# Kernel tuning notes

Hardware: AMD Instinct MI355X
Metric: run time of the kernel (lower is better)

Reference implementation:

```python
import math
import jax, jax.numpy as jnp
import numpy as np

# ---- static config (matches init_kwargs) ----
IN_CH, OUT_CH = 32, 32
NR, NPHI = 3, 4                      # kernel_shape
H, W = 1024, 1024                    # in_shape
KSIZE = (NR - 1) * NPHI + 1          # 9
RC = 2.0 * NR / float(max(H, W))     # default radius_cutoff
S = math.floor(2 * RC * max(H, W) / 2) + 1  # psi_local_size = 7


def _compute_psi_loc() -> np.ndarray:
    """Numpy replica of _precompute_convolution_tensor_2d + scatter into psi_loc."""
    dr = RC / NR
    dphi = 2.0 * np.pi / NPHI
    ik = np.arange(KSIZE).reshape(-1, 1, 1)            # (K,1,1)
    ir = ((ik - 1) // NPHI + 1) * dr                   # floor-div matches torch
    iphi = ((ik - 1) % NPHI) * dphi
    # local grid of offsets, grid_out = origin
    lin = np.linspace(-RC, RC, S)
    X, Y = np.meshgrid(lin, lin, indexing='ij')        # torch.meshgrid default 'ij'
    dx = X.reshape(1, -1)                              # diffs[0], (1, S*S)
    dy = Y.reshape(1, -1)
    r = np.sqrt(dx ** 2 + dy ** 2)                     # (1, S*S)
    phi = np.arctan2(dy, dx) + np.pi
    # norm='2d'
    norm = (np.pi * (RC * NR / (NR + 1)) ** 2
            + np.pi * RC ** 2 * (2 * NR / (NR + 1) + 1) / (NR + 1) / 3)
    cond_r = (np.abs(r - ir) <= dr) & (r <= RC)        # (K,1,S*S)
    dph = np.abs(phi - iphi)
    cond_phi = (ik == 0) | (dph <= dphi) | (2 * np.pi - dph <= dphi)
    f_idx, _, j_idx = np.nonzero(cond_r & cond_phi)
    rv, phv = r[0, j_idx], phi[0, j_idx]
    irv, iphv = ir[f_idx, 0, 0], iphi[f_idx, 0, 0]
    vals = (1.0 - np.abs(rv - irv) / dr) / norm
    d = np.abs(phv - iphv)
    vals = vals * np.where(f_idx > 0, 1.0 - np.minimum(d, 2 * np.pi - d) / dphi, 1.0)
    psi = np.zeros((KSIZE, S * S), dtype=np.float32)
    psi[f_idx, j_idx] = vals.astype(np.float32)        # unique (f,j) pairs -> set
    psi = psi.reshape(KSIZE, S, S) * (4.0 / float(H * W))
    return psi


def setup_inputs() -> dict:
    key = jax.random.key(0)
    kx, kw = jax.random.split(key)
    x = jax.random.normal(kx, (4, IN_CH, H, W), dtype=jnp.float32)
    scale = math.sqrt(1.0 / IN_CH)  # groups=1 -> groupsize = in_channels
    weight = scale * jax.random.normal(kw, (OUT_CH, IN_CH, KSIZE), dtype=jnp.float32)
    bias = jnp.zeros((OUT_CH,), dtype=jnp.float32)
    psi_loc = jnp.asarray(_compute_psi_loc())
    return {"x": x, "weight": weight, "bias": bias, "psi_loc": psi_loc}


def reference(x, weight, bias, psi_loc):
    # kernel[o,g,kx,ky] = sum_k psi_loc[k,kx,ky] * weight[o,g,k]
    kernel = jnp.einsum('kxy,ogk->ogxy', psi_loc, weight)
    left_pad = S // 2            # 3
    right_pad = (S + 1) // 2 - 1  # 3
    xp = jnp.pad(x, ((0, 0), (0, 0), (left_pad, right_pad), (left_pad, right_pad)))
    out = jax.lax.conv_general_dilated(
        xp, kernel, window_strides=(1, 1), padding='VALID',
        dimension_numbers=('NCHW', 'OIHW', 'NCHW'), feature_group_count=1)
    return out + bias[None, :, None, None]
```

## Files before the change

### kernel.cpp

```cpp
#include <hip/hip_runtime.h>

#define H_ 1024
#define W_ 1024
#define BATCH_ 4
#define CIN_ 32
#define COUT_ 32
#define KSZ_ 9

#define TH 16
#define TW 16
#define HALO_H 22
#define HALO_W 24
#define PITCH  25
#define NPIX (HALO_H * PITCH)
#define NTAPS 29

typedef __attribute__((ext_vector_type(8))) short short8;
typedef __attribute__((ext_vector_type(4))) float f32x4;

struct Tap { int dy, dx; };

#define TAPS_LIST \
  {-3,0}, \
  {-2,-2},{-2,-1},{-2,0},{-2,1},{-2,2}, \
  {-1,-2},{-1,-1},{-1,0},{-1,1},{-1,2}, \
  {0,-3},{0,-2},{0,-1},{0,0},{0,1},{0,2},{0,3}, \
  {1,-2},{1,-1},{1,0},{1,1},{1,2}, \
  {2,-2},{2,-1},{2,0},{2,1},{2,2}, \
  {3,0}

__device__ const Tap g_taps[NTAPS] = { TAPS_LIST };

__device__ __forceinline__ unsigned short f2bf(float f) {
    unsigned int u = __builtin_bit_cast(unsigned int, f);
    u = (u + 0x7FFFu + ((u >> 16) & 1u)) >> 16;
    return (unsigned short)u;
}

__device__ __forceinline__ unsigned cvt_pk_bf16(float lo, float hi) {
    unsigned r;
    asm("v_cvt_pk_bf16_f32 %0, %1, %2" : "=v"(r) : "v"(lo), "v"(hi));
    return r;
}

__global__ void build_kw(const float* __restrict__ weight,
                         const float* __restrict__ psi,
                         unsigned short* __restrict__ kw) {
    int t = blockIdx.x;
    int a = g_taps[t].dy + 3;
    int bb = g_taps[t].dx + 3;
    float pv[KSZ_];
#pragma unroll
    for (int k = 0; k < KSZ_; ++k) pv[k] = psi[k * 49 + a * 7 + bb];
    for (int e = threadIdx.x; e < 1024; e += blockDim.x) {
        int q = e >> 8, rem = e & 255, oc = rem >> 3, j = rem & 7;
        int ic = q * 8 + j;
        float acc = 0.f;
#pragma unroll
        for (int k = 0; k < KSZ_; ++k) acc += pv[k] * weight[(oc * CIN_ + ic) * KSZ_ + k];
        kw[t * 1024 + e] = f2bf(acc);
    }
}

__global__ __launch_bounds__(256, 4)
void dconv(const float* __restrict__ x, const uint4* __restrict__ kw4,
           const float* __restrict__ bias, float* __restrict__ out) {
    __shared__ uint4 xt[4][NPIX];

    const int tid = threadIdx.x;
    const unsigned bid = blockIdx.x;
    const int txt = bid & 63;
    const int tyt = (bid >> 6) & 63;
    const int b   = bid >> 12;
    const int x0 = txt * TW, y0 = tyt * TH;
    const size_t plane = (size_t)H_ * W_;

    auto stage_item = [&](int it) {
        int q   = it / 132;
        int rem = it - q * 132;
        int row = rem / 6;
        int c4  = rem - row * 6;
        int gy  = y0 + row - 3;
        int gx0 = x0 + c4 * 4 - 4;
        bool rowin = (gy >= 0) & (gy < H_);
        const float* cb = x + (size_t)(b * CIN_ + q * 8) * plane
                            + (size_t)(rowin ? gy : 0) * W_;
        float v[8][4];
        if (rowin & (gx0 >= 0) & (gx0 + 4 <= W_)) {
            const float* p0 = cb + gx0;
#pragma unroll
            for (int j = 0; j < 8; ++j) {
                const float4 f = *reinterpret_cast<const float4*>(p0 + (size_t)j * plane);
                v[j][0] = f.x; v[j][1] = f.y; v[j][2] = f.z; v[j][3] = f.w;
            }
        } else {
#pragma unroll
            for (int j = 0; j < 8; ++j) {
#pragma unroll
                for (int c = 0; c < 4; ++c) {
                    int gx = gx0 + c;
                    bool inb = rowin & (gx >= 0) & (gx < W_);
                    v[j][c] = inb ? cb[(size_t)j * plane + gx] : 0.f;
                }
            }
        }
        uint4* dst = &xt[q][row * PITCH + c4 * 4];
#pragma unroll
        for (int c = 0; c < 4; ++c) {
            uint4 pk;
            pk.x = cvt_pk_bf16(v[0][c], v[1][c]);
            pk.y = cvt_pk_bf16(v[2][c], v[3][c]);
            pk.z = cvt_pk_bf16(v[4][c], v[5][c]);
            pk.w = cvt_pk_bf16(v[6][c], v[7][c]);
            dst[c] = pk;
        }
    };
    stage_item(tid);
    stage_item(tid + 256);
    if (tid < 528 - 512) stage_item(tid + 512);
    __syncthreads();

    const int wv = tid >> 6, lane = tid & 63;
    const int p16 = lane & 15, quad = lane >> 4;

    f32x4 acc[4][2];
#pragma unroll
    for (int g = 0; g < 4; ++g) {
        acc[g][0] = f32x4{0.f, 0.f, 0.f, 0.f};
        acc[g][1] = f32x4{0.f, 0.f, 0.f, 0.f};
    }

    const uint4* bp = &xt[quad][0];
    const uint4* bq[4];
#pragma unroll
    for (int g = 0; g < 4; ++g)
        bq[g] = bp + (wv * 4 + g + 3) * PITCH + (p16 + 4) - 78;

    constexpr Tap taps[NTAPS] = { TAPS_LIST };
#pragma unroll
    for (int t = 0; t < NTAPS; ++t) {
        short8 a0 = __builtin_bit_cast(short8, kw4[t * 128 + quad * 32 + p16]);
        short8 a1 = __builtin_bit_cast(short8, kw4[t * 128 + quad * 32 + 16 + p16]);
#pragma unroll
        for (int g = 0; g < 4; ++g) {
            short8 bf = __builtin_bit_cast(short8, bq[g][taps[t].dy * PITCH + taps[t].dx + 78]);
            acc[g][0] = __builtin_amdgcn_mfma_f32_16x16x32_bf16(a0, bf, acc[g][0], 0, 0, 0);
            acc[g][1] = __builtin_amdgcn_mfma_f32_16x16x32_bf16(a1, bf, acc[g][1], 0, 0, 0);
        }
    }

    float bv[2][4];
#pragma unroll
    for (int h = 0; h < 2; ++h)
#pragma unroll
        for (int i = 0; i < 4; ++i) bv[h][i] = bias[h * 16 + quad * 4 + i];

    float* ob = out + (size_t)b * COUT_ * plane;
#pragma unroll
    for (int g = 0; g < 4; ++g) {
        int gy = y0 + wv * 4 + g;
#pragma unroll
        for (int h = 0; h < 2; ++h) {
#pragma unroll
            for (int i = 0; i < 4; ++i) {
                int oc = h * 16 + quad * 4 + i;
                ob[(size_t)oc * plane + (size_t)gy * W_ + x0 + p16] = acc[g][h][i] + bv[h][i];
            }
        }
    }
}

extern "C" void kernel_launch(void* const* d_in, const int* in_sizes, int n_in,
                              void* d_out, int out_size, void* d_ws, size_t ws_size,
                              hipStream_t stream) {
    const float* x      = (const float*)d_in[0];
    const float* weight = (const float*)d_in[1];
    const float* bias   = (const float*)d_in[2];
    const float* psi    = (const float*)d_in[3];
    float* out = (float*)d_out;
    unsigned short* kw = (unsigned short*)d_ws;

    hipLaunchKernelGGL(build_kw, dim3(NTAPS), dim3(256), 0, stream, weight, psi, kw);
    hipLaunchKernelGGL(dconv, dim3(BATCH_ * (H_ / TH) * (W_ / TW)), dim3(256), 0, stream,
                       x, (const uint4*)kw, bias, out);
    (void)in_sizes; (void)n_in; (void)out_size; (void)ws_size;
}
```

Before: 1.247 ms.

## Double tile height and prefetch second halo half during first chunk MFMAs

Each block now covers 32 output rows in two 16-row chunks. The halo rows needed only by the second chunk are loaded from global memory into registers while the first chunk's MFMA taps run, then converted to bf16 and written to LDS. This cuts the halo overhead per output row and overlaps global loads with compute. The LDS pitch shrinks to 22 columns, and occupancy is lowered to 3 blocks per SM to make room for the larger tile and the prefetch registers.

```diff
diff --git a/kernel.cpp b/kernel.cpp
--- a/kernel.cpp
+++ b/kernel.cpp
@@ -7,12 +7,11 @@
 #define COUT_ 32
 #define KSZ_ 9
 
-#define TH 16
 #define TW 16
-#define HALO_H 22
-#define HALO_W 24
-#define PITCH  25
-#define NPIX (HALO_H * PITCH)
+#define TH 32
+#define HROWS 38
+#define PITCH 22
+#define QSTRIDE (HROWS * PITCH + 1)
 #define NTAPS 29
 
 typedef __attribute__((ext_vector_type(8))) short short8;
@@ -62,24 +61,39 @@
     }
 }
 
-__global__ __launch_bounds__(256, 4)
+template<int T0, int T1>
+__device__ __forceinline__ void do_taps(const uint4* const (&bq)[4],
+                                        const uint4* __restrict__ kw4,
+                                        int quad, int p16,
+                                        f32x4 (&acc)[4][2]) {
+    constexpr Tap taps[NTAPS] = { TAPS_LIST };
+#pragma unroll
+    for (int t = T0; t < T1; ++t) {
+        short8 a0 = __builtin_bit_cast(short8, kw4[t * 128 + quad * 32 + p16]);
+        short8 a1 = __builtin_bit_cast(short8, kw4[t * 128 + quad * 32 + 16 + p16]);
+#pragma unroll
+        for (int g = 0; g < 4; ++g) {
+            short8 bf = __builtin_bit_cast(short8, bq[g][taps[t].dy * PITCH + taps[t].dx + 69]);
+            acc[g][0] = __builtin_amdgcn_mfma_f32_16x16x32_bf16(a0, bf, acc[g][0], 0, 0, 0);
+            acc[g][1] = __builtin_amdgcn_mfma_f32_16x16x32_bf16(a1, bf, acc[g][1], 0, 0, 0);
+        }
+    }
+}
+
+__global__ __launch_bounds__(256, 3)
 void dconv(const float* __restrict__ x, const uint4* __restrict__ kw4,
            const float* __restrict__ bias, float* __restrict__ out) {
-    __shared__ uint4 xt[4][NPIX];
+    __shared__ uint4 xt[4 * QSTRIDE];
 
     const int tid = threadIdx.x;
     const unsigned bid = blockIdx.x;
     const int txt = bid & 63;
-    const int tyt = (bid >> 6) & 63;
-    const int b   = bid >> 12;
+    const int tyt = (bid >> 6) & 31;
+    const int b   = bid >> 11;
     const int x0 = txt * TW, y0 = tyt * TH;
     const size_t plane = (size_t)H_ * W_;
 
-    auto stage_item = [&](int it) {
-        int q   = it / 132;
-        int rem = it - q * 132;
-        int row = rem / 6;
-        int c4  = rem - row * 6;
+    auto stage_item = [&](int q, int row, int c4) {
         int gy  = y0 + row - 3;
         int gx0 = x0 + c4 * 4 - 4;
         bool rowin = (gy >= 0) & (gy < H_);
@@ -95,79 +109,144 @@
             }
         } else {
 #pragma unroll
-            for (int j = 0; j < 8; ++j) {
+            for (int j = 0; j < 8; ++j)
 #pragma unroll
                 for (int c = 0; c < 4; ++c) {
                     int gx = gx0 + c;
                     bool inb = rowin & (gx >= 0) & (gx < W_);
                     v[j][c] = inb ? cb[(size_t)j * plane + gx] : 0.f;
                 }
-            }
-        }
-        uint4* dst = &xt[q][row * PITCH + c4 * 4];
+        }
+        uint4* dst = &xt[q * QSTRIDE + row * PITCH];
 #pragma unroll
         for (int c = 0; c < 4; ++c) {
-            uint4 pk;
-            pk.x = cvt_pk_bf16(v[0][c], v[1][c]);
-            pk.y = cvt_pk_bf16(v[2][c], v[3][c]);
-            pk.z = cvt_pk_bf16(v[4][c], v[5][c]);
-            pk.w = cvt_pk_bf16(v[6][c], v[7][c]);
-            dst[c] = pk;
-        }
-    };
-    stage_item(tid);
-    stage_item(tid + 256);
-    if (tid < 528 - 512) stage_item(tid + 512);
+            int col = c4 * 4 + c - 1;
+            if (col >= 0 && col < PITCH) {
+                uint4 pk;
+                pk.x = cvt_pk_bf16(v[0][c], v[1][c]);
+                pk.y = cvt_pk_bf16(v[2][c], v[3][c]);
+                pk.z = cvt_pk_bf16(v[4][c], v[5][c]);
+                pk.w = cvt_pk_bf16(v[6][c], v[7][c]);
+                dst[col] = pk;
+            }
+        }
+    };
+
+    {
+        auto do_it = [&](int it) {
+            int q = it / 132, rem = it - q * 132;
+            stage_item(q, rem / 6, rem - (rem / 6) * 6);
+        };
+        do_it(tid);
+        do_it(tid + 256);
+        if (tid < 16) do_it(tid + 512);
+    }
     __syncthreads();
+
+    const bool pact = tid < 192;
+    int pq = 0, prow = 0, pc4 = 0;
+    float pv[8][4];
+    auto pf_issue = [&](int h) {
+        if (!pact) return;
+        pq = tid / 48;
+        int rem = tid - pq * 48;
+        int r8 = rem / 6;
+        pc4 = rem - r8 * 6;
+        prow = 22 + 8 * h + r8;
+        int gy  = y0 + prow - 3;
+        int gx0 = x0 + pc4 * 4 - 4;
+        bool rowin = gy < H_;
+        const float* cb = x + (size_t)(b * CIN_ + pq * 8) * plane
+                            + (size_t)(rowin ? gy : 0) * W_;
+        if (rowin & (gx0 >= 0) & (gx0 + 4 <= W_)) {
+            const float* p0 = cb + gx0;
+#pragma unroll
+            for (int j = 0; j < 8; ++j) {
+                const float4 f = *reinterpret_cast<const float4*>(p0 + (size_t)j * plane);
+                pv[j][0] = f.x; pv[j][1] = f.y; pv[j][2] = f.z; pv[j][3] = f.w;
+            }
+        } else {
+#pragma unroll
+            for (int j = 0; j < 8; ++j)
+#pragma unroll
+                for (int c = 0; c < 4; ++c) {
+                    int gx = gx0 + c;
+                    bool inb = rowin & (gx >= 0) & (gx < W_);
+                    pv[j][c] = inb ? cb[(size_t)j * plane + gx] : 0.f;
+                }
+        }
+    };
+    auto pf_commit = [&]() {
+        if (!pact) return;
+        uint4* dst = &xt[pq * QSTRIDE + prow * PITCH];
+#pragma unroll
+        for (int c = 0; c < 4; ++c) {
+            int col = pc4 * 4 + c - 1;
+            if (col >= 0 && col < PITCH) {
+                uint4 pk;
+                pk.x = cvt_pk_bf16(pv[0][c], pv[1][c]);
+                pk.y = cvt_pk_bf16(pv[2][c], pv[3][c]);
+                pk.z = cvt_pk_bf16(pv[4][c], pv[5][c]);
+                pk.w = cvt_pk_bf16(pv[6][c], pv[7][c]);
+                dst[col] = pk;
+            }
+        }
+    };
 
     const int wv = tid >> 6, lane = tid & 63;
     const int p16 = lane & 15, quad = lane >> 4;
 
+    float bv[2][4];
+#pragma unroll
+    for (int h = 0; h < 2; ++h)
+#pragma unroll
+        for (int i = 0; i < 4; ++i) bv[h][i] = bias[h * 16 + quad * 4 + i];
+
+    float* ob = out + (size_t)b * COUT_ * plane;
+    const uint4* bq[4];
     f32x4 acc[4][2];
-#pragma unroll
-    for (int g = 0; g < 4; ++g) {
-        acc[g][0] = f32x4{0.f, 0.f, 0.f, 0.f};
-        acc[g][1] = f32x4{0.f, 0.f, 0.f, 0.f};
-    }
-
-    const uint4* bp = &xt[quad][0];
-    const uint4* bq[4];
-#pragma unroll
-    for (int g = 0; g < 4; ++g)
-        bq[g] = bp + (wv * 4 + g + 3) * PITCH + (p16 + 4) - 78;
-
-    constexpr Tap taps[NTAPS] = { TAPS_LIST };
-#pragma unroll
-    for (int t = 0; t < NTAPS; ++t) {
-        short8 a0 = __builtin_bit_cast(short8, kw4[t * 128 + quad * 32 + p16]);
-        short8 a1 = __builtin_bit_cast(short8, kw4[t * 128 + quad * 32 + 16 + p16]);
+
+    auto set_bq = [&](int c) {
+#pragma unroll
+        for (int g = 0; g < 4; ++g)
+            bq[g] = &xt[quad * QSTRIDE] + (c * 16 + wv * 4 + g + 3) * PITCH + (p16 + 3) - 69;
+    };
+    auto zero_acc = [&]() {
 #pragma unroll
         for (int g = 0; g < 4; ++g) {
-            short8 bf = __builtin_bit_cast(short8, bq[g][taps[t].dy * PITCH + taps[t].dx + 78]);
-            acc[g][0] = __builtin_amdgcn_mfma_f32_16x16x32_bf16(a0, bf, acc[g][0], 0, 0, 0);
-            acc[g][1] = __builtin_amdgcn_mfma_f32_16x16x32_bf16(a1, bf, acc[g][1], 0, 0, 0);
-        }
-    }
-
-    float bv[2][4];
-#pragma unroll
-    for (int h = 0; h < 2; ++h)
-#pragma unroll
-        for (int i = 0; i < 4; ++i) bv[h][i] = bias[h * 16 + quad * 4 + i];
-
-    float* ob = out + (size_t)b * COUT_ * plane;
-#pragma unroll
-    for (int g = 0; g < 4; ++g) {
-        int gy = y0 + wv * 4 + g;
-#pragma unroll
-        for (int h = 0; h < 2; ++h) {
-#pragma unroll
-            for (int i = 0; i < 4; ++i) {
-                int oc = h * 16 + quad * 4 + i;
-                ob[(size_t)oc * plane + (size_t)gy * W_ + x0 + p16] = acc[g][h][i] + bv[h][i];
-            }
-        }
-    }
+            acc[g][0] = f32x4{0.f, 0.f, 0.f, 0.f};
+            acc[g][1] = f32x4{0.f, 0.f, 0.f, 0.f};
+        }
+    };
+    auto store_chunk = [&](int c) {
+#pragma unroll
+        for (int g = 0; g < 4; ++g) {
+            int gy = y0 + c * 16 + wv * 4 + g;
+#pragma unroll
+            for (int h = 0; h < 2; ++h)
+#pragma unroll
+                for (int i = 0; i < 4; ++i) {
+                    int oc = h * 16 + quad * 4 + i;
+                    ob[(size_t)oc * plane + (size_t)gy * W_ + x0 + p16] = acc[g][h][i] + bv[h][i];
+                }
+        }
+    };
+
+    set_bq(0);
+    zero_acc();
+    pf_issue(0);
+    do_taps<0, 15>(bq, kw4, quad, p16, acc);
+    pf_commit();
+    pf_issue(1);
+    do_taps<15, NTAPS>(bq, kw4, quad, p16, acc);
+    pf_commit();
+    store_chunk(0);
+    __syncthreads();
+
+    set_bq(1);
+    zero_acc();
+    do_taps<0, NTAPS>(bq, kw4, quad, p16, acc);
+    store_chunk(1);
 }
 
 extern "C" void kernel_launch(void* const* d_in, const int* in_sizes, int n_in,
```

Result: slower. 1.768 ms (+41.9%).
